# Kernel optimization log

Hardware: AMD Instinct MI355X
Metric: run time of the kernel (lower is better)

## Reference

```python
import jax, jax.numpy as jnp
import numpy as np


def _gcn_conv(x, src, dst, norm, W, b, n_nodes):
    # PyG GCNConv: transform then normalized scatter-add aggregation.
    h = x @ W                                        # [N, F_out]
    msg = h[src] * norm[:, None]                     # [E+N, F_out] gather
    out = jax.ops.segment_sum(msg, dst, num_segments=n_nodes)  # scatter-add
    return out + b


def setup_inputs() -> dict:
    key = jax.random.key(0)
    ks = jax.random.split(key, 8)
    N, E, F_in, H, C = 100000, 1000000, 128, 64, 40
    x = jax.random.normal(ks[0], (N, F_in), dtype=jnp.float32)
    edge_index = jax.random.randint(ks[1], (2, E), 0, N, dtype=jnp.int64)
    W1 = jax.random.normal(ks[2], (F_in, H), dtype=jnp.float32) * (1.0 / np.sqrt(F_in))
    b1 = jnp.zeros((H,), jnp.float32)
    W2 = jax.random.normal(ks[3], (H, H), dtype=jnp.float32) * (1.0 / np.sqrt(H))
    b2 = jnp.zeros((H,), jnp.float32)
    Wc = jax.random.normal(ks[4], (H, C), dtype=jnp.float32) * (1.0 / np.sqrt(H))
    bc = jnp.zeros((C,), jnp.float32)
    return {"x": x, "edge_index": edge_index, "W1": W1, "b1": b1,
            "W2": W2, "b2": b2, "Wc": Wc, "bc": bc}


def reference(x, edge_index, W1, b1, W2, b2, Wc, bc):
    n_nodes = x.shape[0]
    # Add self loops (GCNConv default), symmetric normalization.
    loop = jnp.arange(n_nodes, dtype=edge_index.dtype)
    src = jnp.concatenate([edge_index[0], loop])
    dst = jnp.concatenate([edge_index[1], loop])
    deg = jax.ops.segment_sum(jnp.ones_like(dst, jnp.float32), dst,
                              num_segments=n_nodes)
    dinv = jnp.where(deg > 0, jax.lax.rsqrt(jnp.maximum(deg, 1.0)), 0.0)
    norm = dinv[src] * dinv[dst]                     # [E+N]

    h = jax.nn.relu(_gcn_conv(x, src, dst, norm, W1, b1, n_nodes))
    # dropout: identity (inference / training=False)
    h = jax.nn.relu(_gcn_conv(h, src, dst, norm, W2, b2, n_nodes))
    return h @ Wc + bc                               # [N, out_dim]
```

## Files before the change

### kernel.cpp

```cpp
#include <hip/hip_runtime.h>
#include <hip/hip_fp16.h>


#define BUCKET_BITS  8
#define BUCKET_NODES 256
#define MAXB 512
#define CAP  8192
#define OFF_MASK 0x3FFFFF

union H8 { uint4 u; __half h[8]; };
union H4 { uint2 u; __half h[4]; };

__global__ void zero_kernel(int* __restrict__ p, int n) {
    int i = blockIdx.x * blockDim.x + threadIdx.x;
    if (i < n) p[i] = 0;
}

__global__ __launch_bounds__(256) void bucket_fill_kernel(const int* __restrict__ src,
                                                          const int* __restrict__ dst,
                                                          int* __restrict__ bucketCursor,
                                                          unsigned int* __restrict__ bucketArr,
                                                          int E, int NB) {
    __shared__ int lcnt[MAXB];
    __shared__ int dcache[4096];
    for (int i = threadIdx.x; i < NB; i += 256) lcnt[i] = 0;
    __syncthreads();
    const int base = blockIdx.x * 4096;
#pragma unroll
    for (int k = 0; k < 16; ++k) {
        int idx = k * 256 + threadIdx.x;
        int e = base + idx;
        if (e < E) {
            int d = dst[e];
            dcache[idx] = d;
            atomicAdd(&lcnt[d >> BUCKET_BITS], 1);
        }
    }
    __syncthreads();
    for (int i = threadIdx.x; i < NB; i += 256) {
        int c = lcnt[i];
        if (c) lcnt[i] = i * CAP + atomicAdd(&bucketCursor[i], c);
    }
    __syncthreads();
#pragma unroll
    for (int k = 0; k < 16; ++k) {
        int idx = k * 256 + threadIdx.x;
        int e = base + idx;
        if (e < E) {
            int d = dcache[idx];
            int s = src[e];
            int pos = atomicAdd(&lcnt[d >> BUCKET_BITS], 1);
            bucketArr[pos] = ((unsigned)(d & (BUCKET_NODES - 1)) << 24) | (unsigned)s;
        }
    }
}

__global__ __launch_bounds__(256) void node_sort_kernel(const unsigned int* __restrict__ bucketArr,
                                                        const int* __restrict__ bucketCursor,
                                                        unsigned int* __restrict__ nodeInfo,
                                                        float* __restrict__ dinv,
                                                        unsigned int* __restrict__ adj, int N) {
    __shared__ int cnt[BUCKET_NODES];
    __shared__ int scn[BUCKET_NODES];
    __shared__ int cur[BUCKET_NODES];
    const int t = threadIdx.x;
    const int b = blockIdx.x;
    cnt[t] = 0;
    __syncthreads();
    const int e0 = b * CAP;
    const int e1 = e0 + bucketCursor[b];
    for (int e = e0 + t; e < e1; e += 256)
        atomicAdd(&cnt[bucketArr[e] >> 24], 1);
    __syncthreads();
    int v = cnt[t];
    scn[t] = v;
    __syncthreads();
    for (int off = 1; off < 256; off <<= 1) {
        int u = (t >= off) ? scn[t - off] : 0;
        __syncthreads();
        scn[t] += u;
        __syncthreads();
    }
    const int excl = scn[t] - v;
    const int node = b * BUCKET_NODES + t;
    if (node < N) {
        nodeInfo[node] = ((unsigned)v << 22) | (unsigned)(e0 + excl);
        dinv[node]     = rsqrtf((float)(v + 1));
    }
    cur[t] = e0 + excl;
    __syncthreads();
    for (int e = e0 + t; e < e1; e += 256) {
        unsigned int entry = bucketArr[e];
        int pos = atomicAdd(&cur[entry >> 24], 1);
        adj[pos] = entry & 0xFFFFFF;
    }
}

template <int K, int NOUT, bool BIAS, bool AHALF, bool OHALF, bool SCALE>
__global__ __launch_bounds__(256) void gemm_tiled(const void* __restrict__ Av,
                                                  const float* __restrict__ W,
                                                  const float* __restrict__ bias,
                                                  const float* __restrict__ dscale,
                                                  void* __restrict__ outv, int M) {
    constexpr int KS  = 64;
    constexpr int NST = K / KS;
    __shared__ float At[64 * 66];
    __shared__ float Wt[K * 64];

    for (int i = threadIdx.x; i < K * 64; i += 256) {
        if (NOUT == 64) {
            Wt[i] = W[i];
        } else {
            int k = i >> 6, c = i & 63;
            Wt[i] = (c < NOUT) ? W[k * NOUT + c] : 0.f;
        }
    }

    const int tc   = threadIdx.x & 15;
    const int tr   = threadIdx.x >> 4;
    const int row0 = blockIdx.x * 64;

    float acc[4][4] = {};

    for (int st = 0; st < NST; ++st) {
        __syncthreads();
        if (AHALF) {
            const __half* Ah = (const __half*)Av;
            int g = threadIdx.x;
#pragma unroll
            for (int i = 0; i < 2; ++i, g += 256) {
                int r  = g >> 3;
                int kc = (g & 7) << 3;
                int grow = row0 + r;
                if (grow > M - 1) grow = M - 1;
                H8 v;
                v.u = *(const uint4*)(Ah + (size_t)grow * K + st * KS + kc);
                float* p = &At[r * 66 + kc];
#pragma unroll
                for (int j = 0; j < 8; ++j) p[j] = __half2float(v.h[j]);
            }
        } else {
            const float* Af = (const float*)Av;
            int g = threadIdx.x;
#pragma unroll
            for (int i = 0; i < 4; ++i, g += 256) {
                int r  = g >> 4;
                int kc = (g & 15) << 2;
                int grow = row0 + r;
                if (grow > M - 1) grow = M - 1;
                float4 v = *(const float4*)(Af + (size_t)grow * K + st * KS + kc);
                float* p = &At[r * 66 + kc];
                p[0] = v.x; p[1] = v.y; p[2] = v.z; p[3] = v.w;
            }
        }
        __syncthreads();

        const float* a0p = &At[(tr * 4 + 0) * 66];
        const float* a1p = &At[(tr * 4 + 1) * 66];
        const float* a2p = &At[(tr * 4 + 2) * 66];
        const float* a3p = &At[(tr * 4 + 3) * 66];
        const float* wp  = &Wt[st * KS * 64 + tc * 4];
#pragma unroll 8
        for (int k = 0; k < KS; ++k) {
            float a0 = a0p[k];
            float a1 = a1p[k];
            float a2 = a2p[k];
            float a3 = a3p[k];
            float4 w = *(const float4*)(wp + k * 64);
            acc[0][0] += a0 * w.x; acc[0][1] += a0 * w.y; acc[0][2] += a0 * w.z; acc[0][3] += a0 * w.w;
            acc[1][0] += a1 * w.x; acc[1][1] += a1 * w.y; acc[1][2] += a1 * w.z; acc[1][3] += a1 * w.w;
            acc[2][0] += a2 * w.x; acc[2][1] += a2 * w.y; acc[2][2] += a2 * w.z; acc[2][3] += a2 * w.w;
            acc[3][0] += a3 * w.x; acc[3][1] += a3 * w.y; acc[3][2] += a3 * w.z; acc[3][3] += a3 * w.w;
        }
    }

    if (NOUT < 64 && tc * 4 >= NOUT) return;
    float4 bb = {0.f, 0.f, 0.f, 0.f};
    if (BIAS) bb = *(const float4*)(bias + tc * 4);
#pragma unroll
    for (int j = 0; j < 4; ++j) {
        int row = row0 + tr * 4 + j;
        if (row >= M) break;
        float sc = SCALE ? dscale[row] : 1.f;
        float vx = acc[j][0] * sc + bb.x;
        float vy = acc[j][1] * sc + bb.y;
        float vz = acc[j][2] * sc + bb.z;
        float vw = acc[j][3] * sc + bb.w;
        if (OHALF) {
            __half* oh = (__half*)outv;
            H4 v;
            v.h[0] = __float2half(vx); v.h[1] = __float2half(vy);
            v.h[2] = __float2half(vz); v.h[3] = __float2half(vw);
            *(uint2*)(oh + (size_t)row * NOUT + tc * 4) = v.u;
        } else {
            float4 v = {vx, vy, vz, vw};
            *(float4*)((float*)outv + (size_t)row * NOUT + tc * 4) = v;
        }
    }
}

__global__ __launch_bounds__(256) void gather_kernel(const __half* __restrict__ h,
                                                     const unsigned int* __restrict__ nodeInfo,
                                                     const unsigned int* __restrict__ adj,
                                                     const float* __restrict__ dinv,
                                                     const float* __restrict__ bias,
                                                     __half* __restrict__ out, int N) {
    const int node = blockIdx.x * 32 + (threadIdx.x >> 3);
    const int o    = (threadIdx.x >> 3) & 7;
    const int l    = threadIdx.x & 7;
    if (node >= N) return;

    const unsigned info = nodeInfo[node];
    const int start = (int)(info & OFF_MASK);
    const int end   = start + (int)(info >> 22);
    const float di  = dinv[node];

    float acc[8];
    {
        H8 sv;
        sv.u = *(const uint4*)(h + (size_t)node * 64 + l * 8);
#pragma unroll
        for (int k = 0; k < 8; ++k) acc[k] = __half2float(sv.h[k]);
    }

    for (int base = start; ; base += 8) {
        bool active = base < end;
        if (__ballot(active) == 0ull) break;
        int m = 0;
        int sidx = 0;
        if (active) {
            m = min(8, end - base);
            if (l < m) sidx = (int)adj[base + l];
        }
#pragma unroll
        for (int j = 0; j < 8; ++j) {
            if (j < m) {
                int s = __shfl(sidx, (o << 3) | j);
                H8 rv;
                rv.u = *(const uint4*)(h + (size_t)s * 64 + l * 8);
#pragma unroll
                for (int k = 0; k < 8; ++k) acc[k] += __half2float(rv.h[k]);
            }
        }
    }

    const float4 b0 = *(const float4*)(bias + l * 8);
    const float4 b1 = *(const float4*)(bias + l * 8 + 4);
    const float bb[8] = {b0.x, b0.y, b0.z, b0.w, b1.x, b1.y, b1.z, b1.w};
    H8 ov;
#pragma unroll
    for (int k = 0; k < 8; ++k) {
        float v = acc[k] * di + bb[k];
        ov.h[k] = __float2half(v > 0.f ? v : 0.f);
    }
    *(uint4*)(out + (size_t)node * 64 + l * 8) = ov.u;
}

extern "C" void kernel_launch(void* const* d_in, const int* in_sizes, int n_in,
                              void* d_out, int out_size, void* d_ws, size_t ws_size,
                              hipStream_t stream) {
    const float* x  = (const float*)d_in[0];
    const int*   ei = (const int*)d_in[1];
    const float* W1 = (const float*)d_in[2];
    const float* b1 = (const float*)d_in[3];
    const float* W2 = (const float*)d_in[4];
    const float* b2 = (const float*)d_in[5];
    const float* Wc = (const float*)d_in[6];
    const float* bc = (const float*)d_in[7];

    const int N = in_sizes[0] / 128;
    const int E = in_sizes[1] / 2;
    const int* src = ei;
    const int* dst = ei + E;

    const int NB = (N + BUCKET_NODES - 1) >> BUCKET_BITS;
    const int EB = (E + 4095) / 4096;

    char* w = (char*)d_ws;
    auto alloc = [&](size_t bytes) { char* p = w; w += (bytes + 255) & ~(size_t)255; return p; };
    int*          bucketCursor = (int*)alloc((size_t)NB * 4);
    unsigned int* bucketArr    = (unsigned int*)alloc((size_t)NB * CAP * 4);
    unsigned int* nodeInfo     = (unsigned int*)alloc((size_t)N * 4);
    unsigned int* adj          = (unsigned int*)alloc((size_t)NB * CAP * 4);
    float*        dinv         = (float*)alloc((size_t)N * 4);
    __half*       bufA         = (__half*)alloc((size_t)N * 64 * 2);
    __half*       bufB         = (__half*)alloc((size_t)N * 64 * 2);

    dim3 blk(256);
    const int nblkG = (N + 63) / 64;
    const int nblkV = (N + 31) / 32;

    zero_kernel<<<(NB + 255) / 256, blk, 0, stream>>>(bucketCursor, NB);
    bucket_fill_kernel<<<EB, blk, 0, stream>>>(src, dst, bucketCursor, bucketArr, E, NB);
    node_sort_kernel<<<NB, blk, 0, stream>>>(bucketArr, bucketCursor, nodeInfo, dinv, adj, N);

    gemm_tiled<128, 64, false, false, true, true><<<nblkG, blk, 0, stream>>>(x, W1, nullptr, dinv, bufA, N);
    gather_kernel<<<nblkV, blk, 0, stream>>>(bufA, nodeInfo, adj, dinv, b1, bufB, N);

    gemm_tiled<64, 64, false, true, true, true><<<nblkG, blk, 0, stream>>>(bufB, W2, nullptr, dinv, bufA, N);
    gather_kernel<<<nblkV, blk, 0, stream>>>(bufA, nodeInfo, adj, dinv, b2, bufB, N);

    gemm_tiled<64, 40, true, true, false, false><<<nblkG, blk, 0, stream>>>(bufB, Wc, bc, nullptr, d_out, N);
}
```

Before: 244.8 us.

## Replace FP32 tiled GEMMs with split-fp16 MFMA matrix-core GEMMs

Swaps the three scalar-FMA shared-memory tiled GEMMs for kernels built on the 16x16x32 f16 MFMA instruction. Weights are split into high and low fp16 parts stored transposed in LDS, and fp32 inputs are split the same way, so two or three MFMAs per tile recover near-fp32 accuracy. The A operand is loaded straight from global memory into registers with no LDS staging. This targets GEMM compute time, at the cost of extra MFMAs for precision emulation and narrower, uncoalesced per-element output stores.

Result: faster. 222.2 us (-9.2%).

```diff
diff --git a/kernel.cpp b/kernel.cpp
--- a/kernel.cpp
+++ b/kernel.cpp
@@ -8,8 +8,11 @@
 #define CAP  8192
 #define OFF_MASK 0x3FFFFF
 
-union H8 { uint4 u; __half h[8]; };
-union H4 { uint2 u; __half h[4]; };
+typedef _Float16 half8 __attribute__((ext_vector_type(8)));
+typedef float    f32x4 __attribute__((ext_vector_type(4)));
+
+union H8  { uint4 u; __half h[8]; };
+union HV8 { uint4 u; half8 h; };
 
 __global__ void zero_kernel(int* __restrict__ p, int n) {
     int i = blockIdx.x * blockDim.x + threadIdx.x;
@@ -96,105 +99,83 @@
     }
 }
 
-template <int K, int NOUT, bool BIAS, bool AHALF, bool OHALF, bool SCALE>
-__global__ __launch_bounds__(256) void gemm_tiled(const void* __restrict__ Av,
-                                                  const float* __restrict__ W,
-                                                  const float* __restrict__ bias,
-                                                  const float* __restrict__ dscale,
-                                                  void* __restrict__ outv, int M) {
-    constexpr int KS  = 64;
-    constexpr int NST = K / KS;
-    __shared__ float At[64 * 66];
-    __shared__ float Wt[K * 64];
+template <int K, int NOUT, int NCT, bool AHALF, bool OHALF, bool SCALE, bool BIAS>
+__global__ __launch_bounds__(256) void gemm_mfma(const void* __restrict__ Av,
+                                                 const float* __restrict__ W,
+                                                 const float* __restrict__ bias,
+                                                 const float* __restrict__ dscale,
+                                                 void* __restrict__ outv, int M) {
+    constexpr int KP = K + 8;
+    __shared__ _Float16 WTh[64 * KP];
+    __shared__ _Float16 WTl[64 * KP];
 
     for (int i = threadIdx.x; i < K * 64; i += 256) {
-        if (NOUT == 64) {
-            Wt[i] = W[i];
+        int k = i >> 6, c = i & 63;
+        float w = (NOUT == 64 || c < NOUT) ? W[k * NOUT + c] : 0.f;
+        _Float16 h = (_Float16)w;
+        WTh[c * KP + k] = h;
+        WTl[c * KP + k] = (_Float16)(w - (float)h);
+    }
+    __syncthreads();
+
+    const int lane = threadIdx.x & 63;
+    const int wv   = threadIdx.x >> 6;
+    const int r    = lane & 15;
+    const int q    = lane >> 4;
+    int arow = blockIdx.x * 64 + wv * 16 + r;
+    if (arow > M - 1) arow = M - 1;
+
+    f32x4 acc[NCT] = {};
+
+#pragma unroll
+    for (int kst = 0; kst < K; kst += 32) {
+        half8 ah = {}, al = {};
+        if (AHALF) {
+            HV8 v;
+            v.u = *(const uint4*)((const __half*)Av + (size_t)arow * K + kst + q * 8);
+            ah = v.h;
         } else {
-            int k = i >> 6, c = i & 63;
-            Wt[i] = (c < NOUT) ? W[k * NOUT + c] : 0.f;
-        }
-    }
-
-    const int tc   = threadIdx.x & 15;
-    const int tr   = threadIdx.x >> 4;
-    const int row0 = blockIdx.x * 64;
-
-    float acc[4][4] = {};
-
-    for (int st = 0; st < NST; ++st) {
-        __syncthreads();
-        if (AHALF) {
-            const __half* Ah = (const __half*)Av;
-            int g = threadIdx.x;
-#pragma unroll
-            for (int i = 0; i < 2; ++i, g += 256) {
-                int r  = g >> 3;
-                int kc = (g & 7) << 3;
-                int grow = row0 + r;
-                if (grow > M - 1) grow = M - 1;
-                H8 v;
-                v.u = *(const uint4*)(Ah + (size_t)grow * K + st * KS + kc);
-                float* p = &At[r * 66 + kc];
-#pragma unroll
-                for (int j = 0; j < 8; ++j) p[j] = __half2float(v.h[j]);
+            const float* ap = (const float*)Av + (size_t)arow * K + kst + q * 8;
+            float4 f0 = *(const float4*)ap;
+            float4 f1 = *(const float4*)(ap + 4);
+            float fs[8] = {f0.x, f0.y, f0.z, f0.w, f1.x, f1.y, f1.z, f1.w};
+#pragma unroll
+            for (int j = 0; j < 8; ++j) {
+                _Float16 h = (_Float16)fs[j];
+                ah[j] = h;
+                al[j] = (_Float16)(fs[j] - (float)h);
             }
-        } else {
-            const float* Af = (const float*)Av;
-            int g = threadIdx.x;
-#pragma unroll
-            for (int i = 0; i < 4; ++i, g += 256) {
-                int r  = g >> 4;
-                int kc = (g & 15) << 2;
-                int grow = row0 + r;
-                if (grow > M - 1) grow = M - 1;
-                float4 v = *(const float4*)(Af + (size_t)grow * K + st * KS + kc);
-                float* p = &At[r * 66 + kc];
-                p[0] = v.x; p[1] = v.y; p[2] = v.z; p[3] = v.w;
+        }
+#pragma unroll
+        for (int n = 0; n < NCT; ++n) {
+            const int bo = (n * 16 + r) * KP + kst + q * 8;
+            HV8 bh, bl;
+            bh.u = *(const uint4*)(WTh + bo);
+            bl.u = *(const uint4*)(WTl + bo);
+            acc[n] = __builtin_amdgcn_mfma_f32_16x16x32_f16(ah, bh.h, acc[n], 0, 0, 0);
+            acc[n] = __builtin_amdgcn_mfma_f32_16x16x32_f16(ah, bl.h, acc[n], 0, 0, 0);
+            if (!AHALF)
+                acc[n] = __builtin_amdgcn_mfma_f32_16x16x32_f16(al, bh.h, acc[n], 0, 0, 0);
+        }
+    }
+
+    const int orow0 = blockIdx.x * 64 + wv * 16 + q * 4;
+#pragma unroll
+    for (int n = 0; n < NCT; ++n) {
+        const int col = n * 16 + r;
+        float bb = 0.f;
+        if (BIAS) bb = (col < NOUT) ? bias[col] : 0.f;
+#pragma unroll
+        for (int j = 0; j < 4; ++j) {
+            const int row = orow0 + j;
+            if (row >= M) break;
+            const float sc = SCALE ? dscale[row] : 1.f;
+            const float v = acc[n][j] * sc + bb;
+            if (OHALF) {
+                ((__half*)outv)[(size_t)row * NOUT + col] = __float2half(v);
+            } else if (col < NOUT) {
+                ((float*)outv)[(size_t)row * NOUT + col] = v;
             }
-        }
-        __syncthreads();
-
-        const float* a0p = &At[(tr * 4 + 0) * 66];
-        const float* a1p = &At[(tr * 4 + 1) * 66];
-        const float* a2p = &At[(tr * 4 + 2) * 66];
-        const float* a3p = &At[(tr * 4 + 3) * 66];
-        const float* wp  = &Wt[st * KS * 64 + tc * 4];
-#pragma unroll 8
-        for (int k = 0; k < KS; ++k) {
-            float a0 = a0p[k];
-            float a1 = a1p[k];
-            float a2 = a2p[k];
-            float a3 = a3p[k];
-            float4 w = *(const float4*)(wp + k * 64);
-            acc[0][0] += a0 * w.x; acc[0][1] += a0 * w.y; acc[0][2] += a0 * w.z; acc[0][3] += a0 * w.w;
-            acc[1][0] += a1 * w.x; acc[1][1] += a1 * w.y; acc[1][2] += a1 * w.z; acc[1][3] += a1 * w.w;
-            acc[2][0] += a2 * w.x; acc[2][1] += a2 * w.y; acc[2][2] += a2 * w.z; acc[2][3] += a2 * w.w;
-            acc[3][0] += a3 * w.x; acc[3][1] += a3 * w.y; acc[3][2] += a3 * w.z; acc[3][3] += a3 * w.w;
-        }
-    }
-
-    if (NOUT < 64 && tc * 4 >= NOUT) return;
-    float4 bb = {0.f, 0.f, 0.f, 0.f};
-    if (BIAS) bb = *(const float4*)(bias + tc * 4);
-#pragma unroll
-    for (int j = 0; j < 4; ++j) {
-        int row = row0 + tr * 4 + j;
-        if (row >= M) break;
-        float sc = SCALE ? dscale[row] : 1.f;
-        float vx = acc[j][0] * sc + bb.x;
-        float vy = acc[j][1] * sc + bb.y;
-        float vz = acc[j][2] * sc + bb.z;
-        float vw = acc[j][3] * sc + bb.w;
-        if (OHALF) {
-            __half* oh = (__half*)outv;
-            H4 v;
-            v.h[0] = __float2half(vx); v.h[1] = __float2half(vy);
-            v.h[2] = __float2half(vz); v.h[3] = __float2half(vw);
-            *(uint2*)(oh + (size_t)row * NOUT + tc * 4) = v.u;
-        } else {
-            float4 v = {vx, vy, vz, vw};
-            *(float4*)((float*)outv + (size_t)row * NOUT + tc * 4) = v;
         }
     }
 }
@@ -294,11 +275,14 @@
     bucket_fill_kernel<<<EB, blk, 0, stream>>>(src, dst, bucketCursor, bucketArr, E, NB);
     node_sort_kernel<<<NB, blk, 0, stream>>>(bucketArr, bucketCursor, nodeInfo, dinv, adj, N);
 
-    gemm_tiled<128, 64, false, false, true, true><<<nblkG, blk, 0, stream>>>(x, W1, nullptr, dinv, bufA, N);
+    gemm_mfma<128, 64, 4, false, true, true, false><<<nblkG, blk, 0, stream>>>(
+        x, W1, nullptr, dinv, bufA, N);
     gather_kernel<<<nblkV, blk, 0, stream>>>(bufA, nodeInfo, adj, dinv, b1, bufB, N);
 
-    gemm_tiled<64, 64, false, true, true, true><<<nblkG, blk, 0, stream>>>(bufB, W2, nullptr, dinv, bufA, N);
+    gemm_mfma<64, 64, 4, true, true, true, false><<<nblkG, blk, 0, stream>>>(
+        bufB, W2, nullptr, dinv, bufA, N);
     gather_kernel<<<nblkV, blk, 0, stream>>>(bufA, nodeInfo, adj, dinv, b2, bufB, N);
 
-    gemm_tiled<64, 40, true, true, false, false><<<nblkG, blk, 0, stream>>>(bufB, Wc, bc, nullptr, d_out, N);
-}
+    gemm_mfma<64, 40, 3, true, false, false, true><<<nblkG, blk, 0, stream>>>(
+        bufB, Wc, bc, nullptr, d_out, N);
+}
```
